# Performance work log

Hardware: AMD Instinct MI355X
Metric: run time of the kernel (lower is better)

The kernel has to match this reference:

```python
import jax, jax.numpy as jnp
import numpy as np


def setup_inputs() -> dict:
    key = jax.random.key(0)
    B, H = 8192, 32768
    x = jax.random.normal(key, (B, H), dtype=jnp.float32)
    return {"hidden_preactivation_BH": x, "k": 64}


def reference(hidden_preactivation_BH, k):
    # top-k along last dim, then scatter values back into a zero tensor
    vals_BK, idx_BK = jax.lax.top_k(hidden_preactivation_BH, k)
    B = hidden_preactivation_BH.shape[0]
    rows_B1 = jnp.arange(B)[:, None]
    out_BH = jnp.zeros_like(hidden_preactivation_BH)
    out_BH = out_BH.at[rows_B1, idx_BK].set(vals_BK)
    return out_BH
```

## Files before the change

### kernel.cpp

```cpp
#include <hip/hip_runtime.h>
#include <stdint.h>

#define TPB 1024
#define HSZ 32768
#define NCH 8
#define CHF4 1024
#define NW (TPB / 64)
#define CAP 1024

#define BARRIER() do { \
    asm volatile("s_waitcnt lgkmcnt(0)" ::: "memory"); \
    __builtin_amdgcn_s_barrier(); \
} while (0)

#define WAIT_VM0_BARRIER() do { \
    asm volatile("s_waitcnt vmcnt(0) lgkmcnt(0)" ::: "memory"); \
    __builtin_amdgcn_s_barrier(); \
} while (0)

__device__ __forceinline__ uint32_t f2k(float f) {
    uint32_t u = __float_as_uint(f);
    return u ^ (0x80000000u | (uint32_t)(-(int32_t)(u >> 31)));
}

struct Sm {
    float4 row[NCH * CHF4];
    uint32_t hist[4096];
    uint32_t wtot[NW];
    uint32_t cand_key[CAP];
    uint32_t cand_col[CAP];
    uint32_t bin, rem, eqcnt, ncand, chunk_base;
};

__device__ __forceinline__ void dma_chunk(const float* __restrict__ xrow, Sm& sm,
                                          int c, int t) {
    const uint32_t* g = (const uint32_t*)xrow + (size_t)c * (CHF4 * 4) + (size_t)t * 4;
    uint32_t* l = (uint32_t*)(sm.row + c * CHF4 + t);
    __builtin_amdgcn_global_load_lds(
        (const __attribute__((address_space(1))) uint32_t*)g,
        (__attribute__((address_space(3))) uint32_t*)l,
        16, 0, 0);
}

__device__ __forceinline__ void select4096(Sm& sm, uint32_t need, int t) {
    const int lane = t & 63, wid = t >> 6;
    uint32_t b[4], pt = 0;
#pragma unroll
    for (int jj = 0; jj < 4; ++jj) { b[jj] = sm.hist[t * 4 + jj]; pt += b[jj]; }
    uint32_t pre = pt;
#pragma unroll
    for (int off = 1; off < 64; off <<= 1) {
        uint32_t n = (uint32_t)__shfl_down((int)pre, off, 64);
        if (lane + off < 64) pre += n;
    }
    if (lane == 0) sm.wtot[wid] = pre;
    BARRIER();
    uint32_t wsuf = 0;
    for (int w = wid + 1; w < NW; ++w) wsuf += sm.wtot[w];
    const uint32_t Sincl = pre + wsuf;
    const uint32_t Sexcl = Sincl - pt;
    if (Sexcl < need && Sincl >= need) {
        uint32_t run = Sexcl;
#pragma unroll
        for (int jj = 3; jj >= 0; --jj) {
            if (run + b[jj] >= need) { sm.bin = (uint32_t)(t * 4 + jj); sm.rem = need - run; break; }
            run += b[jj];
        }
    }
    BARRIER();
}

__device__ __forceinline__ void select256(Sm& sm, uint32_t need, int t) {
    const int lane = t & 63, wid = t >> 6;
    uint32_t pt = (t < 256) ? sm.hist[t] : 0u;
    uint32_t pre = pt;
#pragma unroll
    for (int off = 1; off < 64; off <<= 1) {
        uint32_t n = (uint32_t)__shfl_down((int)pre, off, 64);
        if (lane + off < 64) pre += n;
    }
    if (lane == 0) sm.wtot[wid] = pre;
    BARRIER();
    uint32_t wsuf = 0;
    for (int w = wid + 1; w < NW; ++w) wsuf += sm.wtot[w];
    const uint32_t Sincl = pre + wsuf;
    const uint32_t Sexcl = Sincl - pt;
    if (t < 256 && Sexcl < need && Sincl >= need) {
        sm.bin = (uint32_t)t; sm.rem = need - Sexcl; sm.eqcnt = pt;
    }
    BARRIER();
}

__device__ __forceinline__ void process_row(float* __restrict__ outr,
                                            const float* __restrict__ xnext,
                                            uint32_t k, Sm& sm, int t) {
    float4* outr4 = reinterpret_cast<float4*>(outr);

#pragma unroll
    for (int i = 0; i < 4096 / TPB; ++i) sm.hist[i * TPB + t] = 0u;
    if (t == 0) sm.ncand = 0u;
    BARRIER();
#pragma unroll
    for (int c = 0; c < NCH; ++c) {
        float4 v = sm.row[c * CHF4 + t];
        atomicAdd(&sm.hist[f2k(v.x) >> 20], 1u);
        atomicAdd(&sm.hist[f2k(v.y) >> 20], 1u);
        atomicAdd(&sm.hist[f2k(v.z) >> 20], 1u);
        atomicAdd(&sm.hist[f2k(v.w) >> 20], 1u);
    }
    BARRIER();
    select4096(sm, k, t);
    const uint32_t B1 = sm.bin;
    const uint32_t need2 = sm.rem;

#pragma unroll
    for (int c = 0; c < NCH; ++c) {
        float4 v = sm.row[c * CHF4 + t];
        float vals[4] = { v.x, v.y, v.z, v.w };
#pragma unroll
        for (int e = 0; e < 4; ++e) {
            uint32_t key = f2k(vals[e]);
            if ((key >> 20) == B1) {
                uint32_t pos = atomicAdd(&sm.ncand, 1u);
                if (pos < CAP) {
                    sm.cand_key[pos] = key;
                    sm.cand_col[pos] = (uint32_t)((c * CHF4 + t) * 4 + e);
                }
            }
        }
    }
    BARRIER();
    const uint32_t C = sm.ncand;

    uint32_t K, eqneed, eqcnt;
    if (C <= CAP) {
#pragma unroll
        for (int i = 0; i < 4096 / TPB; ++i) sm.hist[i * TPB + t] = 0u;
        BARRIER();
        for (uint32_t i = t; i < C; i += TPB)
            atomicAdd(&sm.hist[(sm.cand_key[i] >> 8) & 0xFFFu], 1u);
        BARRIER();
        select4096(sm, need2, t);
        const uint32_t B2 = sm.bin;
        const uint32_t need3 = sm.rem;

        if (t < 256) sm.hist[t] = 0u;
        BARRIER();
        const uint32_t pref = (B1 << 12) | B2;
        for (uint32_t i = t; i < C; i += TPB)
            if ((sm.cand_key[i] >> 8) == pref) atomicAdd(&sm.hist[sm.cand_key[i] & 0xFFu], 1u);
        BARRIER();
        select256(sm, need3, t);
        K = (pref << 8) | sm.bin;
        eqneed = sm.rem;
        eqcnt = sm.eqcnt;
    } else {
#pragma unroll
        for (int i = 0; i < 4096 / TPB; ++i) sm.hist[i * TPB + t] = 0u;
        BARRIER();
#pragma unroll
        for (int c = 0; c < NCH; ++c) {
            float4 v = sm.row[c * CHF4 + t];
            float vals[4] = { v.x, v.y, v.z, v.w };
#pragma unroll
            for (int e = 0; e < 4; ++e) {
                uint32_t key = f2k(vals[e]);
                if ((key >> 20) == B1) atomicAdd(&sm.hist[(key >> 8) & 0xFFFu], 1u);
            }
        }
        BARRIER();
        select4096(sm, need2, t);
        const uint32_t B2 = sm.bin;
        const uint32_t need3 = sm.rem;

        if (t < 256) sm.hist[t] = 0u;
        BARRIER();
        const uint32_t pref = (B1 << 12) | B2;
#pragma unroll
        for (int c = 0; c < NCH; ++c) {
            float4 v = sm.row[c * CHF4 + t];
            float vals[4] = { v.x, v.y, v.z, v.w };
#pragma unroll
            for (int e = 0; e < 4; ++e) {
                uint32_t key = f2k(vals[e]);
                if ((key >> 8) == pref) atomicAdd(&sm.hist[key & 0xFFu], 1u);
            }
        }
        BARRIER();
        select256(sm, need3, t);
        K = (pref << 8) | sm.bin;
        eqneed = sm.rem;
        eqcnt = sm.eqcnt;
    }

    if (eqcnt == eqneed) {
#pragma unroll
        for (int c = 0; c < NCH; ++c) {
            float4 v = sm.row[c * CHF4 + t];
            float ov[4] = {
                (f2k(v.x) >= K) ? v.x : 0.0f, (f2k(v.y) >= K) ? v.y : 0.0f,
                (f2k(v.z) >= K) ? v.z : 0.0f, (f2k(v.w) >= K) ? v.w : 0.0f };
            BARRIER();
            if (xnext) dma_chunk(xnext, sm, c, t);
            float4 o; o.x = ov[0]; o.y = ov[1]; o.z = ov[2]; o.w = ov[3];
            outr4[c * CHF4 + t] = o;
        }
    } else if (C <= CAP) {
#pragma unroll
        for (int c = 0; c < NCH; ++c) {
            float4 v = sm.row[c * CHF4 + t];
            float vals[4] = { v.x, v.y, v.z, v.w };
            float ov[4];
#pragma unroll
            for (int e = 0; e < 4; ++e) {
                uint32_t key = f2k(vals[e]);
                bool take = key > K;
                if (key == K) {
                    uint32_t col = (uint32_t)((c * CHF4 + t) * 4 + e);
                    uint32_t rank = 0;
                    for (uint32_t m = 0; m < C; ++m)
                        if (sm.cand_key[m] == K && sm.cand_col[m] < col) ++rank;
                    take = (rank < eqneed);
                }
                ov[e] = take ? vals[e] : 0.0f;
            }
            BARRIER();
            if (xnext) dma_chunk(xnext, sm, c, t);
            float4 o; o.x = ov[0]; o.y = ov[1]; o.z = ov[2]; o.w = ov[3];
            outr4[c * CHF4 + t] = o;
        }
    } else {
        if (t == 0) sm.chunk_base = 0u;
        BARRIER();
        const int lane = t & 63;
        const int wid = t >> 6;
        for (int c = 0; c < NCH; ++c) {
            float4 v = sm.row[c * CHF4 + t];
            float vals[4] = { v.x, v.y, v.z, v.w };
            uint32_t keys[4];
            uint32_t e0 = 0;
#pragma unroll
            for (int e = 0; e < 4; ++e) { keys[e] = f2k(vals[e]); e0 += (keys[e] == K) ? 1u : 0u; }
            uint32_t pre = e0;
            for (int off = 1; off < 64; off <<= 1) {
                uint32_t n = (uint32_t)__shfl_up((int)pre, off, 64);
                if (lane >= off) pre += n;
            }
            if (lane == 63) sm.wtot[wid] = pre;
            BARRIER();
            uint32_t before = sm.chunk_base + (pre - e0);
            for (int w = 0; w < wid; ++w) before += sm.wtot[w];
            float ov[4];
#pragma unroll
            for (int e = 0; e < 4; ++e) {
                bool take = keys[e] > K;
                if (keys[e] == K) { take = (before < eqneed); ++before; }
                ov[e] = take ? vals[e] : 0.0f;
            }
            float4 o; o.x = ov[0]; o.y = ov[1]; o.z = ov[2]; o.w = ov[3];
            outr4[c * CHF4 + t] = o;
            BARRIER();
            if (t == 0) {
                uint32_t s2 = sm.chunk_base;
#pragma unroll
                for (int w = 0; w < NW; ++w) s2 += sm.wtot[w];
                sm.chunk_base = s2;
            }
            BARRIER();
        }
        BARRIER();
        if (xnext) {
#pragma unroll
            for (int c = 0; c < NCH; ++c) dma_chunk(xnext, sm, c, t);
        }
    }
}

__global__ __launch_bounds__(TPB) void topk_scatter_kernel(
    const float* __restrict__ x,
    const int* __restrict__ kp,
    float* __restrict__ out,
    int nrows)
{
    __shared__ Sm sm;
    const int t = threadIdx.x;
    const uint32_t k = (uint32_t)kp[0];
    const int gs = (int)gridDim.x;

    if (k == 0u || k >= (uint32_t)HSZ) {
        for (int r = (int)blockIdx.x; r < nrows; r += gs) {
            const float4* xr4 = reinterpret_cast<const float4*>(x + (size_t)r * HSZ);
            float4* outr4 = reinterpret_cast<float4*>(out + (size_t)r * HSZ);
#pragma unroll
            for (int c = 0; c < NCH; ++c) {
                float4 o;
                if (k == 0u) { o.x = o.y = o.z = o.w = 0.0f; }
                else o = xr4[c * CHF4 + t];
                outr4[c * CHF4 + t] = o;
            }
        }
        return;
    }

    int r = (int)blockIdx.x;
    if (r >= nrows) return;

#pragma unroll
    for (int c = 0; c < NCH; ++c) dma_chunk(x + (size_t)r * HSZ, sm, c, t);

    for (;;) {
        WAIT_VM0_BARRIER();
        const int rn = r + gs;
        const float* xnext = (rn < nrows) ? (x + (size_t)rn * HSZ) : nullptr;
        process_row(out + (size_t)r * HSZ, xnext, k, sm, t);
        if (rn >= nrows) break;
        r = rn;
    }
}

extern "C" void kernel_launch(void* const* d_in, const int* in_sizes, int n_in,
                              void* d_out, int out_size, void* d_ws, size_t ws_size,
                              hipStream_t stream) {
    const float* x = (const float*)d_in[0];
    const int* kp = (const int*)d_in[1];
    float* out = (float*)d_out;
    const int total = in_sizes[0];
    const int rows = total / HSZ;
    int grid = rows < 256 ? rows : 256;
    topk_scatter_kernel<<<grid, TPB, 0, stream>>>(x, kp, out, rows);
}
```

Baseline: 551.5 us.

## Write output during candidate pass and scatter boundary-bin survivors afterward

```diff
diff --git a/kernel.cpp b/kernel.cpp
--- a/kernel.cpp
+++ b/kernel.cpp
@@ -21,6 +21,10 @@
 __device__ __forceinline__ uint32_t f2k(float f) {
     uint32_t u = __float_as_uint(f);
     return u ^ (0x80000000u | (uint32_t)(-(int32_t)(u >> 31)));
+}
+__device__ __forceinline__ float k2f(uint32_t key) {
+    uint32_t u = (key & 0x80000000u) ? (key ^ 0x80000000u) : ~key;
+    return __uint_as_float(u);
 }
 
 struct Sm {
@@ -91,7 +95,8 @@
     BARRIER();
 }
 
-__device__ __forceinline__ void process_row(float* __restrict__ outr,
+__device__ __forceinline__ void process_row(const float* __restrict__ xcur,
+                                            float* __restrict__ outr,
                                             const float* __restrict__ xnext,
                                             uint32_t k, Sm& sm, int t) {
     float4* outr4 = reinterpret_cast<float4*>(outr);
@@ -117,10 +122,13 @@
     for (int c = 0; c < NCH; ++c) {
         float4 v = sm.row[c * CHF4 + t];
         float vals[4] = { v.x, v.y, v.z, v.w };
+        float ov[4];
 #pragma unroll
         for (int e = 0; e < 4; ++e) {
             uint32_t key = f2k(vals[e]);
-            if ((key >> 20) == B1) {
+            uint32_t b = key >> 20;
+            ov[e] = (b > B1) ? vals[e] : 0.0f;
+            if (b == B1) {
                 uint32_t pos = atomicAdd(&sm.ncand, 1u);
                 if (pos < CAP) {
                     sm.cand_key[pos] = key;
@@ -128,11 +136,14 @@
                 }
             }
         }
+        BARRIER();
+        if (xnext) dma_chunk(xnext, sm, c, t);
+        float4 o; o.x = ov[0]; o.y = ov[1]; o.z = ov[2]; o.w = ov[3];
+        outr4[c * CHF4 + t] = o;
     }
     BARRIER();
     const uint32_t C = sm.ncand;
 
-    uint32_t K, eqneed, eqcnt;
     if (C <= CAP) {
 #pragma unroll
         for (int i = 0; i < 4096 / TPB; ++i) sm.hist[i * TPB + t] = 0u;
@@ -151,16 +162,36 @@
             if ((sm.cand_key[i] >> 8) == pref) atomicAdd(&sm.hist[sm.cand_key[i] & 0xFFu], 1u);
         BARRIER();
         select256(sm, need3, t);
-        K = (pref << 8) | sm.bin;
-        eqneed = sm.rem;
-        eqcnt = sm.eqcnt;
+        const uint32_t K = (pref << 8) | sm.bin;
+        const uint32_t eqneed = sm.rem;
+        const uint32_t eqcnt = sm.eqcnt;
+
+        WAIT_VM0_BARRIER();
+        if (eqcnt == eqneed) {
+            for (uint32_t i = t; i < C; i += TPB) {
+                uint32_t key = sm.cand_key[i];
+                if (key >= K) outr[sm.cand_col[i]] = k2f(key);
+            }
+        } else {
+            for (uint32_t i = t; i < C; i += TPB) {
+                uint32_t key = sm.cand_key[i];
+                if (key > K) {
+                    outr[sm.cand_col[i]] = k2f(key);
+                } else if (key == K) {
+                    uint32_t rank = 0, col = sm.cand_col[i];
+                    for (uint32_t m = 0; m < C; ++m)
+                        if (sm.cand_key[m] == K && sm.cand_col[m] < col) ++rank;
+                    if (rank < eqneed) outr[sm.cand_col[i]] = k2f(key);
+                }
+            }
+        }
     } else {
+        const float4* xr4 = reinterpret_cast<const float4*>(xcur);
 #pragma unroll
         for (int i = 0; i < 4096 / TPB; ++i) sm.hist[i * TPB + t] = 0u;
         BARRIER();
-#pragma unroll
         for (int c = 0; c < NCH; ++c) {
-            float4 v = sm.row[c * CHF4 + t];
+            float4 v = xr4[c * CHF4 + t];
             float vals[4] = { v.x, v.y, v.z, v.w };
 #pragma unroll
             for (int e = 0; e < 4; ++e) {
@@ -176,9 +207,8 @@
         if (t < 256) sm.hist[t] = 0u;
         BARRIER();
         const uint32_t pref = (B1 << 12) | B2;
-#pragma unroll
         for (int c = 0; c < NCH; ++c) {
-            float4 v = sm.row[c * CHF4 + t];
+            float4 v = xr4[c * CHF4 + t];
             float vals[4] = { v.x, v.y, v.z, v.w };
 #pragma unroll
             for (int e = 0; e < 4; ++e) {
@@ -188,90 +218,59 @@
         }
         BARRIER();
         select256(sm, need3, t);
-        K = (pref << 8) | sm.bin;
-        eqneed = sm.rem;
-        eqcnt = sm.eqcnt;
-    }
-
-    if (eqcnt == eqneed) {
-#pragma unroll
-        for (int c = 0; c < NCH; ++c) {
-            float4 v = sm.row[c * CHF4 + t];
-            float ov[4] = {
-                (f2k(v.x) >= K) ? v.x : 0.0f, (f2k(v.y) >= K) ? v.y : 0.0f,
-                (f2k(v.z) >= K) ? v.z : 0.0f, (f2k(v.w) >= K) ? v.w : 0.0f };
+        const uint32_t K = (pref << 8) | sm.bin;
+        const uint32_t eqneed = sm.rem;
+        const uint32_t eqcnt = sm.eqcnt;
+
+        WAIT_VM0_BARRIER();
+        if (eqcnt == eqneed) {
+            for (int c = 0; c < NCH; ++c) {
+                float4 v = xr4[c * CHF4 + t];
+                float ov[4] = {
+                    (f2k(v.x) >= K) ? v.x : 0.0f, (f2k(v.y) >= K) ? v.y : 0.0f,
+                    (f2k(v.z) >= K) ? v.z : 0.0f, (f2k(v.w) >= K) ? v.w : 0.0f };
+                float4 o; o.x = ov[0]; o.y = ov[1]; o.z = ov[2]; o.w = ov[3];
+                outr4[c * CHF4 + t] = o;
+            }
+        } else {
+            if (t == 0) sm.chunk_base = 0u;
             BARRIER();
-            if (xnext) dma_chunk(xnext, sm, c, t);
-            float4 o; o.x = ov[0]; o.y = ov[1]; o.z = ov[2]; o.w = ov[3];
-            outr4[c * CHF4 + t] = o;
-        }
-    } else if (C <= CAP) {
-#pragma unroll
-        for (int c = 0; c < NCH; ++c) {
-            float4 v = sm.row[c * CHF4 + t];
-            float vals[4] = { v.x, v.y, v.z, v.w };
-            float ov[4];
-#pragma unroll
-            for (int e = 0; e < 4; ++e) {
-                uint32_t key = f2k(vals[e]);
-                bool take = key > K;
-                if (key == K) {
-                    uint32_t col = (uint32_t)((c * CHF4 + t) * 4 + e);
-                    uint32_t rank = 0;
-                    for (uint32_t m = 0; m < C; ++m)
-                        if (sm.cand_key[m] == K && sm.cand_col[m] < col) ++rank;
-                    take = (rank < eqneed);
-                }
-                ov[e] = take ? vals[e] : 0.0f;
-            }
-            BARRIER();
-            if (xnext) dma_chunk(xnext, sm, c, t);
-            float4 o; o.x = ov[0]; o.y = ov[1]; o.z = ov[2]; o.w = ov[3];
-            outr4[c * CHF4 + t] = o;
-        }
-    } else {
-        if (t == 0) sm.chunk_base = 0u;
-        BARRIER();
-        const int lane = t & 63;
-        const int wid = t >> 6;
-        for (int c = 0; c < NCH; ++c) {
-            float4 v = sm.row[c * CHF4 + t];
-            float vals[4] = { v.x, v.y, v.z, v.w };
-            uint32_t keys[4];
-            uint32_t e0 = 0;
-#pragma unroll
-            for (int e = 0; e < 4; ++e) { keys[e] = f2k(vals[e]); e0 += (keys[e] == K) ? 1u : 0u; }
-            uint32_t pre = e0;
-            for (int off = 1; off < 64; off <<= 1) {
-                uint32_t n = (uint32_t)__shfl_up((int)pre, off, 64);
-                if (lane >= off) pre += n;
-            }
-            if (lane == 63) sm.wtot[wid] = pre;
-            BARRIER();
-            uint32_t before = sm.chunk_base + (pre - e0);
-            for (int w = 0; w < wid; ++w) before += sm.wtot[w];
-            float ov[4];
-#pragma unroll
-            for (int e = 0; e < 4; ++e) {
-                bool take = keys[e] > K;
-                if (keys[e] == K) { take = (before < eqneed); ++before; }
-                ov[e] = take ? vals[e] : 0.0f;
-            }
-            float4 o; o.x = ov[0]; o.y = ov[1]; o.z = ov[2]; o.w = ov[3];
-            outr4[c * CHF4 + t] = o;
-            BARRIER();
-            if (t == 0) {
-                uint32_t s2 = sm.chunk_base;
-#pragma unroll
-                for (int w = 0; w < NW; ++w) s2 += sm.wtot[w];
-                sm.chunk_base = s2;
-            }
-            BARRIER();
-        }
-        BARRIER();
-        if (xnext) {
-#pragma unroll
-            for (int c = 0; c < NCH; ++c) dma_chunk(xnext, sm, c, t);
+            const int lane = t & 63;
+            const int wid = t >> 6;
+            for (int c = 0; c < NCH; ++c) {
+                float4 v = xr4[c * CHF4 + t];
+                float vals[4] = { v.x, v.y, v.z, v.w };
+                uint32_t keys[4];
+                uint32_t e0 = 0;
+#pragma unroll
+                for (int e = 0; e < 4; ++e) { keys[e] = f2k(vals[e]); e0 += (keys[e] == K) ? 1u : 0u; }
+                uint32_t pre = e0;
+                for (int off = 1; off < 64; off <<= 1) {
+                    uint32_t n = (uint32_t)__shfl_up((int)pre, off, 64);
+                    if (lane >= off) pre += n;
+                }
+                if (lane == 63) sm.wtot[wid] = pre;
+                BARRIER();
+                uint32_t before = sm.chunk_base + (pre - e0);
+                for (int w = 0; w < wid; ++w) before += sm.wtot[w];
+                float ov[4];
+#pragma unroll
+                for (int e = 0; e < 4; ++e) {
+                    bool take = keys[e] > K;
+                    if (keys[e] == K) { take = (before < eqneed); ++before; }
+                    ov[e] = take ? vals[e] : 0.0f;
+                }
+                float4 o; o.x = ov[0]; o.y = ov[1]; o.z = ov[2]; o.w = ov[3];
+                outr4[c * CHF4 + t] = o;
+                BARRIER();
+                if (t == 0) {
+                    uint32_t s2 = sm.chunk_base;
+#pragma unroll
+                    for (int w = 0; w < NW; ++w) s2 += sm.wtot[w];
+                    sm.chunk_base = s2;
+                }
+                BARRIER();
+            }
         }
     }
 }
@@ -312,7 +311,7 @@
         WAIT_VM0_BARRIER();
         const int rn = r + gs;
         const float* xnext = (rn < nrows) ? (x + (size_t)rn * HSZ) : nullptr;
-        process_row(out + (size_t)r * HSZ, xnext, k, sm, t);
+        process_row(x + (size_t)r * HSZ, out + (size_t)r * HSZ, xnext, k, sm, t);
         if (rn >= nrows) break;
         r = rn;
     }
```

Measured after the change: 580.6 us. 1.05x slower.

## Pipeline histogram with per-chunk DMA waits, double-buffer histograms, bitwise candidate radix

Applied to the files above, without the earlier changes.

```diff
diff --git a/kernel.cpp b/kernel.cpp
--- a/kernel.cpp
+++ b/kernel.cpp
@@ -6,6 +6,7 @@
 #define NCH 8
 #define CHF4 1024
 #define NW (TPB / 64)
+#define NBIN 2048
 #define CAP 1024
 
 #define BARRIER() do { \
@@ -13,9 +14,9 @@
     __builtin_amdgcn_s_barrier(); \
 } while (0)
 
-#define WAIT_VM0_BARRIER() do { \
-    asm volatile("s_waitcnt vmcnt(0) lgkmcnt(0)" ::: "memory"); \
-    __builtin_amdgcn_s_barrier(); \
+#define WAITVM(n) do { \
+    asm volatile("s_waitcnt vmcnt(" #n ")" ::: "memory"); \
+    __builtin_amdgcn_sched_barrier(0); \
 } while (0)
 
 __device__ __forceinline__ uint32_t f2k(float f) {
@@ -25,10 +26,10 @@
 
 struct Sm {
     float4 row[NCH * CHF4];
-    uint32_t hist[4096];
-    uint32_t wtot[NW];
+    uint32_t hist[2][NBIN];
     uint32_t cand_key[CAP];
     uint32_t cand_col[CAP];
+    uint32_t wtot[NW];
     uint32_t bin, rem, eqcnt, ncand, chunk_base;
 };
 
@@ -42,11 +43,11 @@
         16, 0, 0);
 }
 
-__device__ __forceinline__ void select4096(Sm& sm, uint32_t need, int t) {
+__device__ __forceinline__ void select2048(Sm& sm, int h, uint32_t need, int t) {
     const int lane = t & 63, wid = t >> 6;
-    uint32_t b[4], pt = 0;
-#pragma unroll
-    for (int jj = 0; jj < 4; ++jj) { b[jj] = sm.hist[t * 4 + jj]; pt += b[jj]; }
+    const uint32_t b0 = sm.hist[h][t * 2];
+    const uint32_t b1 = sm.hist[h][t * 2 + 1];
+    const uint32_t pt = b0 + b1;
     uint32_t pre = pt;
 #pragma unroll
     for (int off = 1; off < 64; off <<= 1) {
@@ -60,221 +61,19 @@
     const uint32_t Sincl = pre + wsuf;
     const uint32_t Sexcl = Sincl - pt;
     if (Sexcl < need && Sincl >= need) {
-        uint32_t run = Sexcl;
-#pragma unroll
-        for (int jj = 3; jj >= 0; --jj) {
-            if (run + b[jj] >= need) { sm.bin = (uint32_t)(t * 4 + jj); sm.rem = need - run; break; }
-            run += b[jj];
-        }
+        if (Sexcl + b1 >= need) { sm.bin = (uint32_t)(t * 2 + 1); sm.rem = need - Sexcl; sm.eqcnt = b1; }
+        else { sm.bin = (uint32_t)(t * 2); sm.rem = need - Sexcl - b1; sm.eqcnt = b0; }
     }
     BARRIER();
 }
 
-__device__ __forceinline__ void select256(Sm& sm, uint32_t need, int t) {
-    const int lane = t & 63, wid = t >> 6;
-    uint32_t pt = (t < 256) ? sm.hist[t] : 0u;
-    uint32_t pre = pt;
-#pragma unroll
-    for (int off = 1; off < 64; off <<= 1) {
-        uint32_t n = (uint32_t)__shfl_down((int)pre, off, 64);
-        if (lane + off < 64) pre += n;
-    }
-    if (lane == 0) sm.wtot[wid] = pre;
-    BARRIER();
-    uint32_t wsuf = 0;
-    for (int w = wid + 1; w < NW; ++w) wsuf += sm.wtot[w];
-    const uint32_t Sincl = pre + wsuf;
-    const uint32_t Sexcl = Sincl - pt;
-    if (t < 256 && Sexcl < need && Sincl >= need) {
-        sm.bin = (uint32_t)t; sm.rem = need - Sexcl; sm.eqcnt = pt;
-    }
-    BARRIER();
-}
-
-__device__ __forceinline__ void process_row(float* __restrict__ outr,
-                                            const float* __restrict__ xnext,
-                                            uint32_t k, Sm& sm, int t) {
-    float4* outr4 = reinterpret_cast<float4*>(outr);
-
-#pragma unroll
-    for (int i = 0; i < 4096 / TPB; ++i) sm.hist[i * TPB + t] = 0u;
-    if (t == 0) sm.ncand = 0u;
-    BARRIER();
-#pragma unroll
-    for (int c = 0; c < NCH; ++c) {
-        float4 v = sm.row[c * CHF4 + t];
-        atomicAdd(&sm.hist[f2k(v.x) >> 20], 1u);
-        atomicAdd(&sm.hist[f2k(v.y) >> 20], 1u);
-        atomicAdd(&sm.hist[f2k(v.z) >> 20], 1u);
-        atomicAdd(&sm.hist[f2k(v.w) >> 20], 1u);
-    }
-    BARRIER();
-    select4096(sm, k, t);
-    const uint32_t B1 = sm.bin;
-    const uint32_t need2 = sm.rem;
-
-#pragma unroll
-    for (int c = 0; c < NCH; ++c) {
-        float4 v = sm.row[c * CHF4 + t];
-        float vals[4] = { v.x, v.y, v.z, v.w };
-#pragma unroll
-        for (int e = 0; e < 4; ++e) {
-            uint32_t key = f2k(vals[e]);
-            if ((key >> 20) == B1) {
-                uint32_t pos = atomicAdd(&sm.ncand, 1u);
-                if (pos < CAP) {
-                    sm.cand_key[pos] = key;
-                    sm.cand_col[pos] = (uint32_t)((c * CHF4 + t) * 4 + e);
-                }
-            }
-        }
-    }
-    BARRIER();
-    const uint32_t C = sm.ncand;
-
-    uint32_t K, eqneed, eqcnt;
-    if (C <= CAP) {
-#pragma unroll
-        for (int i = 0; i < 4096 / TPB; ++i) sm.hist[i * TPB + t] = 0u;
-        BARRIER();
-        for (uint32_t i = t; i < C; i += TPB)
-            atomicAdd(&sm.hist[(sm.cand_key[i] >> 8) & 0xFFFu], 1u);
-        BARRIER();
-        select4096(sm, need2, t);
-        const uint32_t B2 = sm.bin;
-        const uint32_t need3 = sm.rem;
-
-        if (t < 256) sm.hist[t] = 0u;
-        BARRIER();
-        const uint32_t pref = (B1 << 12) | B2;
-        for (uint32_t i = t; i < C; i += TPB)
-            if ((sm.cand_key[i] >> 8) == pref) atomicAdd(&sm.hist[sm.cand_key[i] & 0xFFu], 1u);
-        BARRIER();
-        select256(sm, need3, t);
-        K = (pref << 8) | sm.bin;
-        eqneed = sm.rem;
-        eqcnt = sm.eqcnt;
-    } else {
-#pragma unroll
-        for (int i = 0; i < 4096 / TPB; ++i) sm.hist[i * TPB + t] = 0u;
-        BARRIER();
-#pragma unroll
-        for (int c = 0; c < NCH; ++c) {
-            float4 v = sm.row[c * CHF4 + t];
-            float vals[4] = { v.x, v.y, v.z, v.w };
-#pragma unroll
-            for (int e = 0; e < 4; ++e) {
-                uint32_t key = f2k(vals[e]);
-                if ((key >> 20) == B1) atomicAdd(&sm.hist[(key >> 8) & 0xFFFu], 1u);
-            }
-        }
-        BARRIER();
-        select4096(sm, need2, t);
-        const uint32_t B2 = sm.bin;
-        const uint32_t need3 = sm.rem;
-
-        if (t < 256) sm.hist[t] = 0u;
-        BARRIER();
-        const uint32_t pref = (B1 << 12) | B2;
-#pragma unroll
-        for (int c = 0; c < NCH; ++c) {
-            float4 v = sm.row[c * CHF4 + t];
-            float vals[4] = { v.x, v.y, v.z, v.w };
-#pragma unroll
-            for (int e = 0; e < 4; ++e) {
-                uint32_t key = f2k(vals[e]);
-                if ((key >> 8) == pref) atomicAdd(&sm.hist[key & 0xFFu], 1u);
-            }
-        }
-        BARRIER();
-        select256(sm, need3, t);
-        K = (pref << 8) | sm.bin;
-        eqneed = sm.rem;
-        eqcnt = sm.eqcnt;
-    }
-
-    if (eqcnt == eqneed) {
-#pragma unroll
-        for (int c = 0; c < NCH; ++c) {
-            float4 v = sm.row[c * CHF4 + t];
-            float ov[4] = {
-                (f2k(v.x) >= K) ? v.x : 0.0f, (f2k(v.y) >= K) ? v.y : 0.0f,
-                (f2k(v.z) >= K) ? v.z : 0.0f, (f2k(v.w) >= K) ? v.w : 0.0f };
-            BARRIER();
-            if (xnext) dma_chunk(xnext, sm, c, t);
-            float4 o; o.x = ov[0]; o.y = ov[1]; o.z = ov[2]; o.w = ov[3];
-            outr4[c * CHF4 + t] = o;
-        }
-    } else if (C <= CAP) {
-#pragma unroll
-        for (int c = 0; c < NCH; ++c) {
-            float4 v = sm.row[c * CHF4 + t];
-            float vals[4] = { v.x, v.y, v.z, v.w };
-            float ov[4];
-#pragma unroll
-            for (int e = 0; e < 4; ++e) {
-                uint32_t key = f2k(vals[e]);
-                bool take = key > K;
-                if (key == K) {
-                    uint32_t col = (uint32_t)((c * CHF4 + t) * 4 + e);
-                    uint32_t rank = 0;
-                    for (uint32_t m = 0; m < C; ++m)
-                        if (sm.cand_key[m] == K && sm.cand_col[m] < col) ++rank;
-                    take = (rank < eqneed);
-                }
-                ov[e] = take ? vals[e] : 0.0f;
-            }
-            BARRIER();
-            if (xnext) dma_chunk(xnext, sm, c, t);
-            float4 o; o.x = ov[0]; o.y = ov[1]; o.z = ov[2]; o.w = ov[3];
-            outr4[c * CHF4 + t] = o;
-        }
-    } else {
-        if (t == 0) sm.chunk_base = 0u;
-        BARRIER();
-        const int lane = t & 63;
-        const int wid = t >> 6;
-        for (int c = 0; c < NCH; ++c) {
-            float4 v = sm.row[c * CHF4 + t];
-            float vals[4] = { v.x, v.y, v.z, v.w };
-            uint32_t keys[4];
-            uint32_t e0 = 0;
-#pragma unroll
-            for (int e = 0; e < 4; ++e) { keys[e] = f2k(vals[e]); e0 += (keys[e] == K) ? 1u : 0u; }
-            uint32_t pre = e0;
-            for (int off = 1; off < 64; off <<= 1) {
-                uint32_t n = (uint32_t)__shfl_up((int)pre, off, 64);
-                if (lane >= off) pre += n;
-            }
-            if (lane == 63) sm.wtot[wid] = pre;
-            BARRIER();
-            uint32_t before = sm.chunk_base + (pre - e0);
-            for (int w = 0; w < wid; ++w) before += sm.wtot[w];
-            float ov[4];
-#pragma unroll
-            for (int e = 0; e < 4; ++e) {
-                bool take = keys[e] > K;
-                if (keys[e] == K) { take = (before < eqneed); ++before; }
-                ov[e] = take ? vals[e] : 0.0f;
-            }
-            float4 o; o.x = ov[0]; o.y = ov[1]; o.z = ov[2]; o.w = ov[3];
-            outr4[c * CHF4 + t] = o;
-            BARRIER();
-            if (t == 0) {
-                uint32_t s2 = sm.chunk_base;
-#pragma unroll
-                for (int w = 0; w < NW; ++w) s2 += sm.wtot[w];
-                sm.chunk_base = s2;
-            }
-            BARRIER();
-        }
-        BARRIER();
-        if (xnext) {
-#pragma unroll
-            for (int c = 0; c < NCH; ++c) dma_chunk(xnext, sm, c, t);
-        }
-    }
-}
+#define A_CHUNK(c) do { \
+    float4 v = sm.row[(c) * CHF4 + t]; \
+    atomicAdd(&sm.hist[hb][f2k(v.x) >> 21], 1u); \
+    atomicAdd(&sm.hist[hb][f2k(v.y) >> 21], 1u); \
+    atomicAdd(&sm.hist[hb][f2k(v.z) >> 21], 1u); \
+    atomicAdd(&sm.hist[hb][f2k(v.w) >> 21], 1u); \
+} while (0)
 
 __global__ __launch_bounds__(TPB) void topk_scatter_kernel(
     const float* __restrict__ x,
@@ -284,37 +83,228 @@
 {
     __shared__ Sm sm;
     const int t = threadIdx.x;
-    const uint32_t k = (uint32_t)kp[0];
     const int gs = (int)gridDim.x;
-
-    if (k == 0u || k >= (uint32_t)HSZ) {
+    const int ki = kp[0];
+
+    if (ki <= 0 || ki >= HSZ) {
         for (int r = (int)blockIdx.x; r < nrows; r += gs) {
             const float4* xr4 = reinterpret_cast<const float4*>(x + (size_t)r * HSZ);
-            float4* outr4 = reinterpret_cast<float4*>(out + (size_t)r * HSZ);
+            float4* o4 = reinterpret_cast<float4*>(out + (size_t)r * HSZ);
 #pragma unroll
             for (int c = 0; c < NCH; ++c) {
                 float4 o;
-                if (k == 0u) { o.x = o.y = o.z = o.w = 0.0f; }
+                if (ki <= 0) { o.x = o.y = o.z = o.w = 0.0f; }
                 else o = xr4[c * CHF4 + t];
-                outr4[c * CHF4 + t] = o;
+                o4[c * CHF4 + t] = o;
             }
         }
         return;
     }
+    const uint32_t k = (uint32_t)ki;
 
     int r = (int)blockIdx.x;
     if (r >= nrows) return;
 
 #pragma unroll
     for (int c = 0; c < NCH; ++c) dma_chunk(x + (size_t)r * HSZ, sm, c, t);
+    for (int i = t; i < 2 * NBIN; i += TPB) ((uint32_t*)sm.hist)[i] = 0u;
+    BARRIER();
+
+    int hb = 0;
+    bool fresh = true;
 
     for (;;) {
-        WAIT_VM0_BARRIER();
+        if (fresh) {
+            WAITVM(7); A_CHUNK(0); WAITVM(6); A_CHUNK(1);
+            WAITVM(5); A_CHUNK(2); WAITVM(4); A_CHUNK(3);
+            WAITVM(3); A_CHUNK(4); WAITVM(2); A_CHUNK(5);
+            WAITVM(1); A_CHUNK(6); WAITVM(0); A_CHUNK(7);
+            fresh = false;
+        } else {
+            WAITVM(14); A_CHUNK(0); WAITVM(12); A_CHUNK(1);
+            WAITVM(10); A_CHUNK(2); WAITVM(8);  A_CHUNK(3);
+            WAITVM(6);  A_CHUNK(4); WAITVM(4);  A_CHUNK(5);
+            WAITVM(2);  A_CHUNK(6); WAITVM(0);  A_CHUNK(7);
+        }
+        BARRIER();
+
+        if (t == 0) sm.ncand = 0u;
+        select2048(sm, hb, k, t);
+        const uint32_t B1 = sm.bin;
+        const uint32_t need2 = sm.rem;
+
+        sm.hist[hb ^ 1][t] = 0u;
+        sm.hist[hb ^ 1][t + TPB] = 0u;
+#pragma unroll
+        for (int c = 0; c < NCH; ++c) {
+            float4 v = sm.row[c * CHF4 + t];
+            float vals[4] = { v.x, v.y, v.z, v.w };
+#pragma unroll
+            for (int e = 0; e < 4; ++e) {
+                uint32_t key = f2k(vals[e]);
+                if ((key >> 21) == B1) {
+                    uint32_t pos = atomicAdd(&sm.ncand, 1u);
+                    if (pos < CAP) {
+                        sm.cand_key[pos] = key;
+                        sm.cand_col[pos] = (uint32_t)((c * CHF4 + t) * 4 + e);
+                    }
+                }
+            }
+        }
+        BARRIER();
+        const uint32_t C = sm.ncand;
+
         const int rn = r + gs;
         const float* xnext = (rn < nrows) ? (x + (size_t)rn * HSZ) : nullptr;
-        process_row(out + (size_t)r * HSZ, xnext, k, sm, t);
+        float4* out4 = reinterpret_cast<float4*>(out + (size_t)r * HSZ);
+
+        if (C <= CAP) {
+            const int lane = t & 63;
+            uint32_t pref = B1 << 21;
+            uint32_t needR = need2;
+            for (int bit = 20; bit >= 0; --bit) {
+                const uint32_t thr = (pref >> bit) | 1u;
+                uint32_t cnt = 0;
+                for (uint32_t i = (uint32_t)lane; i < C; i += 64)
+                    cnt += ((sm.cand_key[i] >> bit) == thr) ? 1u : 0u;
+#pragma unroll
+                for (int off = 32; off; off >>= 1)
+                    cnt += (uint32_t)__shfl_xor((int)cnt, off, 64);
+                if (cnt >= needR) pref |= (1u << bit); else needR -= cnt;
+            }
+            const uint32_t K = pref;
+            const uint32_t eqneed = needR;
+            uint32_t ce = 0;
+            for (uint32_t i = (uint32_t)lane; i < C; i += 64)
+                ce += (sm.cand_key[i] == K) ? 1u : 0u;
+#pragma unroll
+            for (int off = 32; off; off >>= 1)
+                ce += (uint32_t)__shfl_xor((int)ce, off, 64);
+            const bool simple = (ce == eqneed);
+
+#pragma unroll
+            for (int c = 0; c < NCH; ++c) {
+                float4 v = sm.row[c * CHF4 + t];
+                float vals[4] = { v.x, v.y, v.z, v.w };
+                float ov[4];
+#pragma unroll
+                for (int e = 0; e < 4; ++e) {
+                    uint32_t key = f2k(vals[e]);
+                    bool take = key > K;
+                    if (key == K) {
+                        if (simple) take = true;
+                        else {
+                            uint32_t col = (uint32_t)((c * CHF4 + t) * 4 + e);
+                            uint32_t rank = 0;
+                            for (uint32_t m = 0; m < C; ++m)
+                                if (sm.cand_key[m] == K && sm.cand_col[m] < col) ++rank;
+                            take = (rank < eqneed);
+                        }
+                    }
+                    ov[e] = take ? vals[e] : 0.0f;
+                }
+                float4 o; o.x = ov[0]; o.y = ov[1]; o.z = ov[2]; o.w = ov[3];
+                out4[c * CHF4 + t] = o;
+                __builtin_amdgcn_sched_barrier(0);
+                if (xnext) dma_chunk(xnext, sm, c, t);
+                __builtin_amdgcn_sched_barrier(0);
+            }
+        } else {
+#pragma unroll
+            for (int c = 0; c < NCH; ++c) {
+                float4 v = sm.row[c * CHF4 + t];
+                float vals[4] = { v.x, v.y, v.z, v.w };
+#pragma unroll
+                for (int e = 0; e < 4; ++e) {
+                    uint32_t key = f2k(vals[e]);
+                    if ((key >> 21) == B1) atomicAdd(&sm.hist[hb ^ 1][(key >> 10) & 0x7FFu], 1u);
+                }
+            }
+            BARRIER();
+            select2048(sm, hb ^ 1, need2, t);
+            const uint32_t B2b = sm.bin;
+            const uint32_t need3 = sm.rem;
+            sm.hist[hb][t] = 0u; sm.hist[hb][t + TPB] = 0u;
+            BARRIER();
+            const uint32_t pref2 = (B1 << 11) | B2b;
+#pragma unroll
+            for (int c = 0; c < NCH; ++c) {
+                float4 v = sm.row[c * CHF4 + t];
+                float vals[4] = { v.x, v.y, v.z, v.w };
+#pragma unroll
+                for (int e = 0; e < 4; ++e) {
+                    uint32_t key = f2k(vals[e]);
+                    if ((key >> 10) == pref2) atomicAdd(&sm.hist[hb][key & 0x3FFu], 1u);
+                }
+            }
+            BARRIER();
+            select2048(sm, hb, need3, t);
+            const uint32_t K = (pref2 << 10) | sm.bin;
+            const uint32_t eqneed = sm.rem;
+            const uint32_t eqcnt = sm.eqcnt;
+
+            if (eqcnt == eqneed) {
+#pragma unroll
+                for (int c = 0; c < NCH; ++c) {
+                    float4 v = sm.row[c * CHF4 + t];
+                    float ov[4] = {
+                        (f2k(v.x) >= K) ? v.x : 0.0f, (f2k(v.y) >= K) ? v.y : 0.0f,
+                        (f2k(v.z) >= K) ? v.z : 0.0f, (f2k(v.w) >= K) ? v.w : 0.0f };
+                    float4 o; o.x = ov[0]; o.y = ov[1]; o.z = ov[2]; o.w = ov[3];
+                    out4[c * CHF4 + t] = o;
+                }
+            } else {
+                if (t == 0) sm.chunk_base = 0u;
+                BARRIER();
+                const int lane = t & 63;
+                const int wid = t >> 6;
+                for (int c = 0; c < NCH; ++c) {
+                    float4 v = sm.row[c * CHF4 + t];
+                    float vals[4] = { v.x, v.y, v.z, v.w };
+                    uint32_t keys[4];
+                    uint32_t e0 = 0;
+#pragma unroll
+                    for (int e = 0; e < 4; ++e) { keys[e] = f2k(vals[e]); e0 += (keys[e] == K) ? 1u : 0u; }
+                    uint32_t pre = e0;
+                    for (int off = 1; off < 64; off <<= 1) {
+                        uint32_t n = (uint32_t)__shfl_up((int)pre, off, 64);
+                        if (lane >= off) pre += n;
+                    }
+                    if (lane == 63) sm.wtot[wid] = pre;
+                    BARRIER();
+                    uint32_t before = sm.chunk_base + (pre - e0);
+                    for (int w = 0; w < wid; ++w) before += sm.wtot[w];
+                    float ov[4];
+#pragma unroll
+                    for (int e = 0; e < 4; ++e) {
+                        bool take = keys[e] > K;
+                        if (keys[e] == K) { take = (before < eqneed); ++before; }
+                        ov[e] = take ? vals[e] : 0.0f;
+                    }
+                    float4 o; o.x = ov[0]; o.y = ov[1]; o.z = ov[2]; o.w = ov[3];
+                    out4[c * CHF4 + t] = o;
+                    BARRIER();
+                    if (t == 0) {
+                        uint32_t s2 = sm.chunk_base;
+#pragma unroll
+                        for (int w = 0; w < NW; ++w) s2 += sm.wtot[w];
+                        sm.chunk_base = s2;
+                    }
+                    BARRIER();
+                }
+            }
+            if (xnext) {
+#pragma unroll
+                for (int c = 0; c < NCH; ++c) dma_chunk(xnext, sm, c, t);
+            }
+            for (int i = t; i < 2 * NBIN; i += TPB) ((uint32_t*)sm.hist)[i] = 0u;
+            BARRIER();
+            fresh = true;
+        }
+
         if (rn >= nrows) break;
         r = rn;
+        hb ^= 1;
     }
 }
 
```

New measurement: 795.2 us. +44.2%, slower.
